# Optimization experiments

Hardware: AMD Instinct MI355X
Metric: run time of the kernel (lower is better)

The kernel has to match this reference:

```python
import jax, jax.numpy as jnp
import numpy as np
from jax import lax

SHIFT_SIZE = 5
PAD = SHIFT_SIZE // 2


def _chunk_shifts(C):
    # torch.chunk(x, 5, dim=1): chunk size = ceil(C/5); shift for chunk i is i - PAD
    csz = -(-C // SHIFT_SIZE)
    return jnp.arange(C) // csz - PAD  # (C,) in [-PAD, PAD]


def _shift_along_h(x, shifts):
    # x: (B,C,H,W). Equivalent of pad+chunk+roll(dim=2)+cat+narrow: per-channel
    # zero-filled shift along H (no wraparound since |shift| <= PAD).
    B, C, H, W = x.shape
    xp = jnp.pad(x, ((0, 0), (0, 0), (PAD, PAD), (0, 0)))
    c_idx = jnp.arange(C)[:, None]              # (C,1)
    h_idx = jnp.arange(H)[None, :] + PAD - shifts[:, None]  # (C,H)
    return xp[:, c_idx, h_idx, :]               # (B,C,H,W)


def _shift_along_w(x, shifts):
    return jnp.swapaxes(_shift_along_h(jnp.swapaxes(x, 2, 3), shifts), 2, 3)


def setup_inputs() -> dict:
    key = jax.random.key(0)
    ks = jax.random.split(key, 7)
    B, H, W, C, hidden = 8, 128, 128, 256, 256
    x = jax.random.normal(ks[0], (B, H * W, C), dtype=jnp.float32)
    w1 = jax.random.normal(ks[1], (hidden, C), dtype=jnp.float32) * 0.02
    b1 = jnp.zeros((hidden,), dtype=jnp.float32)
    fan_out = 3 * 3 * hidden // hidden  # groups = hidden
    dw_w = jax.random.normal(ks[2], (hidden, 1, 3, 3), dtype=jnp.float32) * np.sqrt(2.0 / fan_out)
    dw_b = jnp.zeros((hidden,), dtype=jnp.float32)
    w2 = jax.random.normal(ks[3], (C, hidden), dtype=jnp.float32) * 0.02
    b2 = jnp.zeros((C,), dtype=jnp.float32)
    return {"x": x, "H": H, "W": W, "w1": w1, "b1": b1,
            "dw_w": dw_w, "dw_b": dw_b, "w2": w2, "b2": b2}


def reference(x, H, W, w1, b1, dw_w, dw_b, w2, b2):
    B, N, C = x.shape
    shifts = _chunk_shifts(C)

    # --- shift along H, then fc1 ---
    xn = jnp.reshape(jnp.swapaxes(x, 1, 2), (B, C, H, W))
    x_s = _shift_along_h(xn, shifts)
    x_s = jnp.swapaxes(x_s.reshape(B, C, H * W), 1, 2)   # (B,N,C)
    h = x_s @ w1.T + b1                                  # (B,N,hidden)

    # --- depthwise 3x3 conv ---
    Ch = h.shape[-1]
    himg = jnp.reshape(jnp.swapaxes(h, 1, 2), (B, Ch, H, W))
    himg = lax.conv_general_dilated(
        himg, dw_w, window_strides=(1, 1), padding=((1, 1), (1, 1)),
        feature_group_count=Ch,
        dimension_numbers=("NCHW", "OIHW", "NCHW")) + dw_b[None, :, None, None]
    h = jnp.swapaxes(himg.reshape(B, Ch, H * W), 1, 2)

    h = jax.nn.gelu(h, approximate=False)

    # --- shift along W, then fc2 ---
    hn = jnp.reshape(jnp.swapaxes(h, 1, 2), (B, Ch, H, W))
    h_s = _shift_along_w(hn, _chunk_shifts(Ch))
    h_s = jnp.swapaxes(h_s.reshape(B, Ch, H * W), 1, 2)  # (B,N,hidden)
    out = h_s @ w2.T + b2                                # (B,N,C)
    return out
```

## Files before the change

### kernel.cpp

```cpp
#include <hip/hip_runtime.h>
#include <hip/hip_bf16.h>
#include <math.h>

#define Hc   128
#define Wc   128
#define Cc   256
#define Nc   (Hc * Wc)
#define Bn   8
#define Mtot (Bn * Nc)
#define CSZ  52
#define SPAD 2

typedef unsigned short ushort4v __attribute__((ext_vector_type(4)));
typedef unsigned short ushort8  __attribute__((ext_vector_type(8)));
typedef __bf16         bf16x8   __attribute__((ext_vector_type(8)));
typedef float          f32x4    __attribute__((ext_vector_type(4)));

__device__ __forceinline__ float bf2f(unsigned short u) {
    return __uint_as_float(((unsigned)u) << 16);
}
__device__ __forceinline__ unsigned short f2bf(float f) {
    unsigned u = __float_as_uint(f);
    return (unsigned short)((u + 0x7fffu + ((u >> 16) & 1u)) >> 16);
}
__device__ __forceinline__ unsigned pk2bf(float a, float b) {
    unsigned ua = __float_as_uint(a) + 0x8000u;
    unsigned ub = __float_as_uint(b) + 0x8000u;
    return __builtin_amdgcn_perm(ub, ua, 0x07060302);
}
__device__ __forceinline__ void async16(const void* g, void* l) {
    __builtin_amdgcn_global_load_lds(
        (const __attribute__((address_space(1))) unsigned*)g,
        (__attribute__((address_space(3))) unsigned*)l, 16, 0, 0);
}

#define FENCE(vm) asm volatile("s_waitcnt vmcnt(" #vm ") lgkmcnt(0)\n\ts_barrier" ::: "memory")

__global__ __launch_bounds__(256)
void shiftwprep_kernel(const float* __restrict__ x, unsigned short* __restrict__ xb,
                       const float* __restrict__ w1, const float* __restrict__ w2,
                       const float* __restrict__ dw_w,
                       unsigned short* __restrict__ w1b, unsigned short* __restrict__ w2b,
                       float* __restrict__ dwT)
{
    const int gid0 = blockIdx.x * 256 + threadIdx.x;
    if (blockIdx.x < 64) {
        const int g = gid0;
        {
            float4 a = *(const float4*)(w1 + (size_t)g * 4);
            ushort4v o = { f2bf(a.x), f2bf(a.y), f2bf(a.z), f2bf(a.w) };
            *(ushort4v*)(w1b + (size_t)g * 4) = o;
        }
        {
            float4 a = *(const float4*)(w2 + (size_t)g * 4);
            ushort4v o = { f2bf(a.x), f2bf(a.y), f2bf(a.z), f2bf(a.w) };
            *(ushort4v*)(w2b + (size_t)g * 4) = o;
        }
        if (g < 9 * Cc) dwT[(g % 9) * Cc + g / 9] = dw_w[g];
    }
#pragma unroll
    for (int it = 0; it < 4; ++it) {
        const int gid = gid0 + it * (4096 * 256);
        const int row = gid >> 5;
        const int c   = (gid & 31) * 8;
        const int hh  = (row >> 7) & 127;
        const int s0  = c / CSZ - SPAD;
        const int s1  = (c + 4) / CSZ - SPAD;
        const int h0  = hh - s0, h1r = hh - s1;
        float4 v0 = make_float4(0.f, 0.f, 0.f, 0.f);
        float4 v1 = make_float4(0.f, 0.f, 0.f, 0.f);
        if (h0  >= 0 && h0  < Hc)
            v0 = *(const float4*)(x + ((size_t)row + (size_t)(h0 - hh) * Wc) * Cc + c);
        if (h1r >= 0 && h1r < Hc)
            v1 = *(const float4*)(x + ((size_t)row + (size_t)(h1r - hh) * Wc) * Cc + c + 4);
        uint4 o;
        o.x = pk2bf(v0.x, v0.y); o.y = pk2bf(v0.z, v0.w);
        o.z = pk2bf(v1.x, v1.y); o.w = pk2bf(v1.z, v1.w);
        *(uint4*)(xb + (size_t)row * Cc + c) = o;
    }
}

__global__ __launch_bounds__(256)
void fc1_mfma_kernel(const unsigned short* __restrict__ xb, const unsigned short* __restrict__ w1b,
                     const float* __restrict__ b1, unsigned short* __restrict__ h1)
{
    __shared__ __align__(16) unsigned char smem[49152];
    __bf16* base = (__bf16*)smem;
    unsigned short* Cs = (unsigned short*)smem;

    const int tid  = threadIdx.x;
    const int lane = tid & 63;
    const int wave = tid >> 6;
    const int wm = (wave >> 1) * 64, wn = (wave & 1) * 64;

    const int lid = ((blockIdx.x & 7) << 8) | (blockIdx.x >> 3);
    const int bx  = lid >> 1;
    const int j0  = (lid & 1) * 128;
    const size_t m0 = (size_t)bx * 128;
    const int idx0 = tid, idx1 = tid + 256;

    const size_t aro0 = (m0 + (idx0 >> 2)) * Cc + (idx0 & 3) * 8;
    const size_t aro1 = (m0 + (idx1 >> 2)) * Cc + (idx1 & 3) * 8;
    const size_t bro0 = (size_t)(j0 + (idx0 >> 2)) * Cc + (idx0 & 3) * 8;
    const size_t bro1 = (size_t)(j0 + (idx1 >> 2)) * Cc + (idx1 & 3) * 8;

    auto stage = [&](int buf, int t) {
        const int k0 = t * 32;
        __bf16* adst = base + buf * 8192;
        __bf16* bdst = adst + 4096;
        async16(xb  + aro0 + k0, adst + idx0 * 8);
        async16(xb  + aro1 + k0, adst + idx1 * 8);
        async16(w1b + bro0 + k0, bdst + idx0 * 8);
        async16(w1b + bro1 + k0, bdst + idx1 * 8);
    };

    f32x4 acc[4][4] = {};
    const int kq = (lane >> 4) * 8;
    const int rr = lane & 15;

    stage(0, 0);
    stage(1, 1);
    FENCE(4);

#define G1_STEP(T, FN)                                                        \
    {                                                                          \
        if constexpr ((T) <= 5) stage(((T) + 2) % 3, (T) + 2);                 \
        bf16x8 a[4], b[4];                                                     \
        const __bf16* ap = base + ((T) % 3) * 8192;                            \
        const __bf16* bp = ap + 4096;                                          \
        _Pragma("unroll")                                                      \
        for (int i = 0; i < 4; ++i) {                                          \
            a[i] = *(const bf16x8*)(ap + (wm + i * 16 + rr) * 32 + kq);        \
            b[i] = *(const bf16x8*)(bp + (wn + i * 16 + rr) * 32 + kq);        \
        }                                                                      \
        _Pragma("unroll")                                                      \
        for (int i = 0; i < 4; ++i)                                            \
            _Pragma("unroll")                                                  \
            for (int j = 0; j < 4; ++j)                                        \
                acc[i][j] = __builtin_amdgcn_mfma_f32_16x16x32_bf16(a[i], b[j], acc[i][j], 0, 0, 0); \
        FN;                                                                    \
    }

    G1_STEP(0, FENCE(4));
    G1_STEP(1, FENCE(4));
    G1_STEP(2, FENCE(4));
    G1_STEP(3, FENCE(4));
    G1_STEP(4, FENCE(4));
    G1_STEP(5, FENCE(4));
    G1_STEP(6, FENCE(0));
    G1_STEP(7, __syncthreads());
#undef G1_STEP

    const int cq = (lane >> 4) * 4;
    const int cc = lane & 15;
    float bv[4];
#pragma unroll
    for (int j = 0; j < 4; ++j) bv[j] = b1[j0 + wn + j * 16 + cc];
#pragma unroll
    for (int i = 0; i < 4; ++i)
#pragma unroll
        for (int j = 0; j < 4; ++j) {
            const int col = wn + j * 16 + cc;
#pragma unroll
            for (int rg = 0; rg < 4; ++rg)
                Cs[(wm + i * 16 + cq + rg) * 136 + col] = f2bf(acc[i][j][rg] + bv[j]);
        }
    __syncthreads();
    {
        const int row = tid >> 1, hf = tid & 1;
        const unsigned short* src = Cs + row * 136 + hf * 64;
        unsigned short* dst = h1 + (m0 + row) * Cc + j0 + hf * 64;
#pragma unroll
        for (int i = 0; i < 8; ++i)
            *(uint4*)(dst + i * 8) = *(const uint4*)(src + i * 8);
    }
}

__global__ __launch_bounds__(256)
void dwconv_gelu_scatter_kernel(const unsigned short* __restrict__ h1,
                                const float* __restrict__ dwT, const float* __restrict__ dw_b,
                                unsigned short* __restrict__ gsh)
{
    const int t   = threadIdx.x;
    const int bh  = blockIdx.x;
    const int bb  = bh >> 7, hh = bh & 127;
    const size_t rowb = (size_t)bb * Nc + (size_t)hh * Wc;

    {
        const int wi = t >> 6;
        const int w  = (wi & 2) ? (wi + 124) : wi;
        const int c8 = (t & 63) * 4;
        uint2 z; z.x = 0u; z.y = 0u;
        *(uint2*)(gsh + (rowb + w) * Cc + c8) = z;
    }
    __syncthreads();

    const int cg  = t & 31;
    const int wq  = t >> 5;
    const int c0  = cg * 8;
    const int s0  = c0 / CSZ - SPAD;
    const int s1  = (c0 + 4) / CSZ - SPAD;

#pragma unroll 1
    for (int qtr = 0; qtr < 4; ++qtr) {
        const int wbase = qtr * 32 + wq * 4 - 1;

        float acc[4][8];
        {
            float4 a0 = *(const float4*)(dw_b + c0);
            float4 a1 = *(const float4*)(dw_b + c0 + 4);
#pragma unroll
            for (int i = 0; i < 4; ++i) {
                acc[i][0] = a0.x; acc[i][1] = a0.y; acc[i][2] = a0.z; acc[i][3] = a0.w;
                acc[i][4] = a1.x; acc[i][5] = a1.y; acc[i][6] = a1.z; acc[i][7] = a1.w;
            }
        }

#pragma unroll
        for (int dy = -1; dy <= 1; ++dy) {
            const int y = hh + dy;
            if (y < 0 || y >= Hc) continue;
            const unsigned short* rp = h1 + ((size_t)bb * Nc + (size_t)y * Wc) * Cc + c0;
            float in[6][8];
#pragma unroll
            for (int dx = 0; dx < 6; ++dx) {
                const int w = wbase + dx;
                ushort8 raw = {0, 0, 0, 0, 0, 0, 0, 0};
                if (w >= 0 && w < Wc) raw = *(const ushort8*)(rp + (size_t)w * Cc);
#pragma unroll
                for (int c = 0; c < 8; ++c) in[dx][c] = bf2f(raw[c]);
            }
            const float* wrow = dwT + (dy + 1) * 3 * Cc + c0;
            float wr[3][8];
#pragma unroll
            for (int tx = 0; tx < 3; ++tx) {
                float4 wa = *(const float4*)(wrow + tx * Cc);
                float4 wb = *(const float4*)(wrow + tx * Cc + 4);
                wr[tx][0] = wa.x; wr[tx][1] = wa.y; wr[tx][2] = wa.z; wr[tx][3] = wa.w;
                wr[tx][4] = wb.x; wr[tx][5] = wb.y; wr[tx][6] = wb.z; wr[tx][7] = wb.w;
            }
#pragma unroll
            for (int i = 0; i < 4; ++i)
#pragma unroll
                for (int tx = 0; tx < 3; ++tx)
#pragma unroll
                    for (int c = 0; c < 8; ++c)
                        acc[i][c] += in[i + tx][c] * wr[tx][c];
        }

#pragma unroll
        for (int i = 0; i < 4; ++i) {
            float g[8];
#pragma unroll
            for (int c = 0; c < 8; ++c) {
                const float v = acc[i][c];
                const float u = v * v;
                const float a = __builtin_fmaf(0.0713548162f, u, 1.5957691216f);
                const float e = __expf(v * a);
                g[c] = v * e * __builtin_amdgcn_rcpf(e + 1.0f);
            }
            uint2 lo, hi;
            lo.x = pk2bf(g[0], g[1]); lo.y = pk2bf(g[2], g[3]);
            hi.x = pk2bf(g[4], g[5]); hi.y = pk2bf(g[6], g[7]);
            const int wo = wbase + 1 + i;
            const int w0 = wo + s0, w1 = wo + s1;
            if ((unsigned)w0 < (unsigned)Wc) *(uint2*)(gsh + (rowb + w0) * Cc + c0)     = lo;
            if ((unsigned)w1 < (unsigned)Wc) *(uint2*)(gsh + (rowb + w1) * Cc + c0 + 4) = hi;
        }
    }
}

__global__ __launch_bounds__(256)
void fc2_mfma_kernel(const unsigned short* __restrict__ A, const unsigned short* __restrict__ w2b,
                     const float* __restrict__ b2, float* __restrict__ out)
{
    __shared__ __align__(16) unsigned char smem[49152];
    __bf16* base = (__bf16*)smem;

    const int tid  = threadIdx.x;
    const int lane = tid & 63;
    const int wave = tid >> 6;
    const int wm = (wave >> 1) * 64, wn = (wave & 1) * 64;

    const int lid = ((blockIdx.x & 7) << 8) | (blockIdx.x >> 3);
    const size_t m0 = (size_t)(lid >> 1) * 128;
    const int j0 = (lid & 1) * 128;
    const int idx0 = tid, idx1 = tid + 256;

    const size_t aro0 = (m0 + (idx0 >> 2)) * Cc + (idx0 & 3) * 8;
    const size_t aro1 = (m0 + (idx1 >> 2)) * Cc + (idx1 & 3) * 8;
    const size_t bro0 = (size_t)(j0 + (idx0 >> 2)) * Cc + (idx0 & 3) * 8;
    const size_t bro1 = (size_t)(j0 + (idx1 >> 2)) * Cc + (idx1 & 3) * 8;

    auto stage = [&](int buf, int t) {
        const int k0 = t * 32;
        __bf16* adst = base + buf * 8192;
        __bf16* bdst = adst + 4096;
        async16(A   + aro0 + k0, adst + idx0 * 8);
        async16(A   + aro1 + k0, adst + idx1 * 8);
        async16(w2b + bro0 + k0, bdst + idx0 * 8);
        async16(w2b + bro1 + k0, bdst + idx1 * 8);
    };

    f32x4 acc[4][4] = {};
    const int kq = (lane >> 4) * 8;
    const int rr = lane & 15;

    stage(0, 0);
    stage(1, 1);
    FENCE(4);

#define G2_STEP(T, FN)                                                        \
    {                                                                          \
        if constexpr ((T) <= 5) stage(((T) + 2) % 3, (T) + 2);                 \
        bf16x8 a[4], b[4];                                                     \
        const __bf16* ap = base + ((T) % 3) * 8192;                            \
        const __bf16* bp = ap + 4096;                                          \
        _Pragma("unroll")                                                      \
        for (int i = 0; i < 4; ++i) {                                          \
            a[i] = *(const bf16x8*)(ap + (wm + i * 16 + rr) * 32 + kq);        \
            b[i] = *(const bf16x8*)(bp + (wn + i * 16 + rr) * 32 + kq);        \
        }                                                                      \
        _Pragma("unroll")                                                      \
        for (int i = 0; i < 4; ++i)                                            \
            _Pragma("unroll")                                                  \
            for (int j = 0; j < 4; ++j)                                        \
                acc[i][j] = __builtin_amdgcn_mfma_f32_16x16x32_bf16(a[i], b[j], acc[i][j], 0, 0, 0); \
        FN;                                                                    \
    }

    G2_STEP(0, FENCE(4));
    G2_STEP(1, FENCE(4));
    G2_STEP(2, FENCE(4));
    G2_STEP(3, FENCE(4));
    G2_STEP(4, FENCE(4));
    G2_STEP(5, FENCE(4));
    G2_STEP(6, FENCE(0));
    G2_STEP(7, ;);
#undef G2_STEP

    const int cq = (lane >> 4) * 4;
    const int cc = lane & 15;
    float bv[4];
#pragma unroll
    for (int j = 0; j < 4; ++j) bv[j] = b2[j0 + wn + j * 16 + cc];
#pragma unroll
    for (int i = 0; i < 4; ++i)
#pragma unroll
        for (int j = 0; j < 4; ++j) {
            const int col = j0 + wn + j * 16 + cc;
#pragma unroll
            for (int rg = 0; rg < 4; ++rg)
                out[(m0 + wm + i * 16 + cq + rg) * Cc + col] = acc[i][j][rg] + bv[j];
        }
}

extern "C" void kernel_launch(void* const* d_in, const int* in_sizes, int n_in,
                              void* d_out, int out_size, void* d_ws, size_t ws_size,
                              hipStream_t stream) {
    const float* x    = (const float*)d_in[0];
    const float* w1   = (const float*)d_in[3];
    const float* b1   = (const float*)d_in[4];
    const float* dw_w = (const float*)d_in[5];
    const float* dw_b = (const float*)d_in[6];
    const float* w2   = (const float*)d_in[7];
    const float* b2   = (const float*)d_in[8];
    float* out = (float*)d_out;

    unsigned short* h1  = (unsigned short*)d_ws;
    unsigned short* gsh = h1 + (size_t)Mtot * Cc;
    unsigned short* w1b = gsh + (size_t)Mtot * Cc;
    unsigned short* w2b = w1b + 65536;
    float*          dwT = (float*)(w2b + 65536);

    shiftwprep_kernel<<<dim3(4096), dim3(256), 0, stream>>>(x, gsh, w1, w2, dw_w, w1b, w2b, dwT);
    fc1_mfma_kernel<<<dim3(2 * Mtot / 128), dim3(256), 0, stream>>>(gsh, w1b, b1, h1);
    dwconv_gelu_scatter_kernel<<<dim3(Mtot / 128), dim3(256), 0, stream>>>(h1, dwT, dw_b, gsh);
    fc2_mfma_kernel<<<dim3(2 * Mtot / 128), dim3(256), 0, stream>>>(gsh, w2b, b2, out);
}
```

Baseline: 350.2 us.

## Widen GEMM tiles to full N=256 and XOR-swizzle LDS staging

Both fc1 and fc2 GEMM kernels now compute a 128x256 output tile per block, so each block covers all output columns. This halves the grid and means the A operand is loaded from global memory only once instead of twice. The LDS layout for A and B is XOR-swizzled on 16-byte chunks to reduce bank conflicts on the fragment reads. The trade-off is twice the accumulator registers (4x8 f32x4 per wave) and 72KB of LDS per block, which lowers occupancy; the fc1 epilogue now writes its output in two passes through the LDS buffer.

```diff
diff --git a/kernel.cpp b/kernel.cpp
--- a/kernel.cpp
+++ b/kernel.cpp
@@ -84,95 +84,110 @@
 void fc1_mfma_kernel(const unsigned short* __restrict__ xb, const unsigned short* __restrict__ w1b,
                      const float* __restrict__ b1, unsigned short* __restrict__ h1)
 {
-    __shared__ __align__(16) unsigned char smem[49152];
-    __bf16* base = (__bf16*)smem;
-    unsigned short* Cs = (unsigned short*)smem;
+    __shared__ __align__(16) unsigned char sm[73728];
+    unsigned short* Cs = (unsigned short*)sm;
 
     const int tid  = threadIdx.x;
     const int lane = tid & 63;
     const int wave = tid >> 6;
-    const int wm = (wave >> 1) * 64, wn = (wave & 1) * 64;
-
-    const int lid = ((blockIdx.x & 7) << 8) | (blockIdx.x >> 3);
-    const int bx  = lid >> 1;
-    const int j0  = (lid & 1) * 128;
-    const size_t m0 = (size_t)bx * 128;
-    const int idx0 = tid, idx1 = tid + 256;
-
-    const size_t aro0 = (m0 + (idx0 >> 2)) * Cc + (idx0 & 3) * 8;
-    const size_t aro1 = (m0 + (idx1 >> 2)) * Cc + (idx1 & 3) * 8;
-    const size_t bro0 = (size_t)(j0 + (idx0 >> 2)) * Cc + (idx0 & 3) * 8;
-    const size_t bro1 = (size_t)(j0 + (idx1 >> 2)) * Cc + (idx1 & 3) * 8;
+    const int wm = (wave >> 1) * 64;
+    const int wn = (wave & 1) * 128;
+
+    const int lid = ((blockIdx.x & 7) << 7) | (blockIdx.x >> 3);
+    const size_t m0 = (size_t)lid * 128;
+
+    const int qa0 = tid, qa1 = tid + 256;
+    const int ra0 = qa0 >> 2, ra1 = qa1 >> 2;
+    const size_t aof0 = (m0 + ra0) * Cc + (((qa0 & 3) ^ (ra0 & 3)) << 3);
+    const size_t aof1 = (m0 + ra1) * Cc + (((qa1 & 3) ^ (ra1 & 3)) << 3);
+    const int qb0 = tid, qb1 = tid + 256, qb2 = tid + 512, qb3 = tid + 768;
+    const int rb0 = qb0 >> 2, rb1 = qb1 >> 2, rb2 = qb2 >> 2, rb3 = qb3 >> 2;
+    const int bof0 = rb0 * Cc + (((qb0 & 3) ^ (rb0 & 3)) << 3);
+    const int bof1 = rb1 * Cc + (((qb1 & 3) ^ (rb1 & 3)) << 3);
+    const int bof2 = rb2 * Cc + (((qb2 & 3) ^ (rb2 & 3)) << 3);
+    const int bof3 = rb3 * Cc + (((qb3 & 3) ^ (rb3 & 3)) << 3);
 
     auto stage = [&](int buf, int t) {
         const int k0 = t * 32;
-        __bf16* adst = base + buf * 8192;
-        __bf16* bdst = adst + 4096;
-        async16(xb  + aro0 + k0, adst + idx0 * 8);
-        async16(xb  + aro1 + k0, adst + idx1 * 8);
-        async16(w1b + bro0 + k0, bdst + idx0 * 8);
-        async16(w1b + bro1 + k0, bdst + idx1 * 8);
+        unsigned char* ad = sm + buf * 24576;
+        unsigned char* bd = ad + 8192;
+        async16(xb  + aof0 + k0, ad + qa0 * 16);
+        async16(xb  + aof1 + k0, ad + qa1 * 16);
+        async16(w1b + bof0 + k0, bd + qb0 * 16);
+        async16(w1b + bof1 + k0, bd + qb1 * 16);
+        async16(w1b + bof2 + k0, bd + qb2 * 16);
+        async16(w1b + bof3 + k0, bd + qb3 * 16);
     };
 
-    f32x4 acc[4][4] = {};
-    const int kq = (lane >> 4) * 8;
-    const int rr = lane & 15;
+    f32x4 acc[4][8] = {};
+    const int rr  = lane & 15;
+    const int axo = (((lane >> 4) ^ (rr & 3)) << 3);
 
     stage(0, 0);
     stage(1, 1);
-    FENCE(4);
+    FENCE(6);
 
 #define G1_STEP(T, FN)                                                        \
     {                                                                          \
         if constexpr ((T) <= 5) stage(((T) + 2) % 3, (T) + 2);                 \
-        bf16x8 a[4], b[4];                                                     \
-        const __bf16* ap = base + ((T) % 3) * 8192;                            \
-        const __bf16* bp = ap + 4096;                                          \
-        _Pragma("unroll")                                                      \
-        for (int i = 0; i < 4; ++i) {                                          \
-            a[i] = *(const bf16x8*)(ap + (wm + i * 16 + rr) * 32 + kq);        \
-            b[i] = *(const bf16x8*)(bp + (wn + i * 16 + rr) * 32 + kq);        \
-        }                                                                      \
+        const __bf16* ap = (const __bf16*)(sm + ((T) % 3) * 24576);            \
+        const __bf16* bp = (const __bf16*)(sm + ((T) % 3) * 24576 + 8192);     \
+        bf16x8 a[4];                                                           \
         _Pragma("unroll")                                                      \
         for (int i = 0; i < 4; ++i)                                            \
+            a[i] = *(const bf16x8*)(ap + (wm + i * 16 + rr) * 32 + axo);       \
+        _Pragma("unroll")                                                      \
+        for (int jh = 0; jh < 2; ++jh) {                                       \
+            bf16x8 b[4];                                                       \
             _Pragma("unroll")                                                  \
             for (int j = 0; j < 4; ++j)                                        \
-                acc[i][j] = __builtin_amdgcn_mfma_f32_16x16x32_bf16(a[i], b[j], acc[i][j], 0, 0, 0); \
+                b[j] = *(const bf16x8*)(bp + (wn + jh * 64 + j * 16 + rr) * 32 + axo); \
+            _Pragma("unroll")                                                  \
+            for (int i = 0; i < 4; ++i)                                        \
+                _Pragma("unroll")                                              \
+                for (int j = 0; j < 4; ++j)                                    \
+                    acc[i][jh * 4 + j] = __builtin_amdgcn_mfma_f32_16x16x32_bf16(a[i], b[j], acc[i][jh * 4 + j], 0, 0, 0); \
+        }                                                                      \
         FN;                                                                    \
     }
 
-    G1_STEP(0, FENCE(4));
-    G1_STEP(1, FENCE(4));
-    G1_STEP(2, FENCE(4));
-    G1_STEP(3, FENCE(4));
-    G1_STEP(4, FENCE(4));
-    G1_STEP(5, FENCE(4));
+    G1_STEP(0, FENCE(6));
+    G1_STEP(1, FENCE(6));
+    G1_STEP(2, FENCE(6));
+    G1_STEP(3, FENCE(6));
+    G1_STEP(4, FENCE(6));
+    G1_STEP(5, FENCE(6));
     G1_STEP(6, FENCE(0));
-    G1_STEP(7, __syncthreads());
+    G1_STEP(7, ;);
 #undef G1_STEP
 
-    const int cq = (lane >> 4) * 4;
-    const int cc = lane & 15;
-    float bv[4];
-#pragma unroll
-    for (int j = 0; j < 4; ++j) bv[j] = b1[j0 + wn + j * 16 + cc];
-#pragma unroll
-    for (int i = 0; i < 4; ++i)
-#pragma unroll
-        for (int j = 0; j < 4; ++j) {
-            const int col = wn + j * 16 + cc;
-#pragma unroll
-            for (int rg = 0; rg < 4; ++rg)
-                Cs[(wm + i * 16 + cq + rg) * 136 + col] = f2bf(acc[i][j][rg] + bv[j]);
-        }
-    __syncthreads();
-    {
-        const int row = tid >> 1, hf = tid & 1;
-        const unsigned short* src = Cs + row * 136 + hf * 64;
-        unsigned short* dst = h1 + (m0 + row) * Cc + j0 + hf * 64;
-#pragma unroll
-        for (int i = 0; i < 8; ++i)
-            *(uint4*)(dst + i * 8) = *(const uint4*)(src + i * 8);
+    const int cq  = (lane >> 4) * 4;
+    const int cc  = lane & 15;
+    const int lcb = wn >> 1;
+#pragma unroll
+    for (int p = 0; p < 2; ++p) {
+        __syncthreads();
+        float bv[4];
+#pragma unroll
+        for (int j = 0; j < 4; ++j) bv[j] = b1[wn + p * 64 + j * 16 + cc];
+#pragma unroll
+        for (int i = 0; i < 4; ++i)
+#pragma unroll
+            for (int j = 0; j < 4; ++j) {
+                const int col = lcb + j * 16 + cc;
+#pragma unroll
+                for (int rg = 0; rg < 4; ++rg)
+                    Cs[(wm + i * 16 + cq + rg) * 136 + col] = f2bf(acc[i][p * 4 + j][rg] + bv[j]);
+            }
+        __syncthreads();
+        {
+            const int row = tid >> 1, hf = tid & 1;
+            const unsigned short* src = Cs + row * 136 + hf * 64;
+            unsigned short* dst = h1 + (m0 + row) * Cc + (hf * 2 + p) * 64;
+#pragma unroll
+            for (int i = 0; i < 8; ++i)
+                *(uint4*)(dst + i * 8) = *(const uint4*)(src + i * 8);
+        }
     }
 }
 
@@ -274,84 +289,96 @@
 void fc2_mfma_kernel(const unsigned short* __restrict__ A, const unsigned short* __restrict__ w2b,
                      const float* __restrict__ b2, float* __restrict__ out)
 {
-    __shared__ __align__(16) unsigned char smem[49152];
-    __bf16* base = (__bf16*)smem;
+    __shared__ __align__(16) unsigned char sm[73728];
 
     const int tid  = threadIdx.x;
     const int lane = tid & 63;
     const int wave = tid >> 6;
-    const int wm = (wave >> 1) * 64, wn = (wave & 1) * 64;
-
-    const int lid = ((blockIdx.x & 7) << 8) | (blockIdx.x >> 3);
-    const size_t m0 = (size_t)(lid >> 1) * 128;
-    const int j0 = (lid & 1) * 128;
-    const int idx0 = tid, idx1 = tid + 256;
-
-    const size_t aro0 = (m0 + (idx0 >> 2)) * Cc + (idx0 & 3) * 8;
-    const size_t aro1 = (m0 + (idx1 >> 2)) * Cc + (idx1 & 3) * 8;
-    const size_t bro0 = (size_t)(j0 + (idx0 >> 2)) * Cc + (idx0 & 3) * 8;
-    const size_t bro1 = (size_t)(j0 + (idx1 >> 2)) * Cc + (idx1 & 3) * 8;
+    const int wm = (wave >> 1) * 64;
+    const int wn = (wave & 1) * 128;
+
+    const int lid = ((blockIdx.x & 7) << 7) | (blockIdx.x >> 3);
+    const size_t m0 = (size_t)lid * 128;
+
+    const int qa0 = tid, qa1 = tid + 256;
+    const int ra0 = qa0 >> 2, ra1 = qa1 >> 2;
+    const size_t aof0 = (m0 + ra0) * Cc + (((qa0 & 3) ^ (ra0 & 3)) << 3);
+    const size_t aof1 = (m0 + ra1) * Cc + (((qa1 & 3) ^ (ra1 & 3)) << 3);
+    const int qb0 = tid, qb1 = tid + 256, qb2 = tid + 512, qb3 = tid + 768;
+    const int rb0 = qb0 >> 2, rb1 = qb1 >> 2, rb2 = qb2 >> 2, rb3 = qb3 >> 2;
+    const int bof0 = rb0 * Cc + (((qb0 & 3) ^ (rb0 & 3)) << 3);
+    const int bof1 = rb1 * Cc + (((qb1 & 3) ^ (rb1 & 3)) << 3);
+    const int bof2 = rb2 * Cc + (((qb2 & 3) ^ (rb2 & 3)) << 3);
+    const int bof3 = rb3 * Cc + (((qb3 & 3) ^ (rb3 & 3)) << 3);
 
     auto stage = [&](int buf, int t) {
         const int k0 = t * 32;
-        __bf16* adst = base + buf * 8192;
-        __bf16* bdst = adst + 4096;
-        async16(A   + aro0 + k0, adst + idx0 * 8);
-        async16(A   + aro1 + k0, adst + idx1 * 8);
-        async16(w2b + bro0 + k0, bdst + idx0 * 8);
-        async16(w2b + bro1 + k0, bdst + idx1 * 8);
+        unsigned char* ad = sm + buf * 24576;
+        unsigned char* bd = ad + 8192;
+        async16(A   + aof0 + k0, ad + qa0 * 16);
+        async16(A   + aof1 + k0, ad + qa1 * 16);
+        async16(w2b + bof0 + k0, bd + qb0 * 16);
+        async16(w2b + bof1 + k0, bd + qb1 * 16);
+        async16(w2b + bof2 + k0, bd + qb2 * 16);
+        async16(w2b + bof3 + k0, bd + qb3 * 16);
     };
 
-    f32x4 acc[4][4] = {};
-    const int kq = (lane >> 4) * 8;
-    const int rr = lane & 15;
+    f32x4 acc[4][8] = {};
+    const int rr  = lane & 15;
+    const int axo = (((lane >> 4) ^ (rr & 3)) << 3);
 
     stage(0, 0);
     stage(1, 1);
-    FENCE(4);
+    FENCE(6);
 
 #define G2_STEP(T, FN)                                                        \
     {                                                                          \
         if constexpr ((T) <= 5) stage(((T) + 2) % 3, (T) + 2);                 \
-        bf16x8 a[4], b[4];                                                     \
-        const __bf16* ap = base + ((T) % 3) * 8192;                            \
-        const __bf16* bp = ap + 4096;                                          \
-        _Pragma("unroll")                                                      \
-        for (int i = 0; i < 4; ++i) {                                          \
-            a[i] = *(const bf16x8*)(ap + (wm + i * 16 + rr) * 32 + kq);        \
-            b[i] = *(const bf16x8*)(bp + (wn + i * 16 + rr) * 32 + kq);        \
-        }                                                                      \
+        const __bf16* ap = (const __bf16*)(sm + ((T) % 3) * 24576);            \
+        const __bf16* bp = (const __bf16*)(sm + ((T) % 3) * 24576 + 8192);     \
+        bf16x8 a[4];                                                           \
         _Pragma("unroll")                                                      \
         for (int i = 0; i < 4; ++i)                                            \
+            a[i] = *(const bf16x8*)(ap + (wm + i * 16 + rr) * 32 + axo);       \
+        _Pragma("unroll")                                                      \
+        for (int jh = 0; jh < 2; ++jh) {                                       \
+            bf16x8 b[4];                                                       \
             _Pragma("unroll")                                                  \
             for (int j = 0; j < 4; ++j)                                        \
-                acc[i][j] = __builtin_amdgcn_mfma_f32_16x16x32_bf16(a[i], b[j], acc[i][j], 0, 0, 0); \
+                b[j] = *(const bf16x8*)(bp + (wn + jh * 64 + j * 16 + rr) * 32 + axo); \
+            _Pragma("unroll")                                                  \
+            for (int i = 0; i < 4; ++i)                                        \
+                _Pragma("unroll")                                              \
+                for (int j = 0; j < 4; ++j)                                    \
+                    acc[i][jh * 4 + j] = __builtin_amdgcn_mfma_f32_16x16x32_bf16(a[i], b[j], acc[i][jh * 4 + j], 0, 0, 0); \
+        }                                                                      \
         FN;                                                                    \
     }
 
-    G2_STEP(0, FENCE(4));
-    G2_STEP(1, FENCE(4));
-    G2_STEP(2, FENCE(4));
-    G2_STEP(3, FENCE(4));
-    G2_STEP(4, FENCE(4));
-    G2_STEP(5, FENCE(4));
+    G2_STEP(0, FENCE(6));
+    G2_STEP(1, FENCE(6));
+    G2_STEP(2, FENCE(6));
+    G2_STEP(3, FENCE(6));
+    G2_STEP(4, FENCE(6));
+    G2_STEP(5, FENCE(6));
     G2_STEP(6, FENCE(0));
     G2_STEP(7, ;);
 #undef G2_STEP
 
     const int cq = (lane >> 4) * 4;
     const int cc = lane & 15;
-    float bv[4];
-#pragma unroll
-    for (int j = 0; j < 4; ++j) bv[j] = b2[j0 + wn + j * 16 + cc];
+    float bv[8];
+#pragma unroll
+    for (int jj = 0; jj < 8; ++jj)
+        bv[jj] = b2[wn + (jj >> 2) * 64 + (jj & 3) * 16 + cc];
 #pragma unroll
     for (int i = 0; i < 4; ++i)
 #pragma unroll
-        for (int j = 0; j < 4; ++j) {
-            const int col = j0 + wn + j * 16 + cc;
+        for (int jj = 0; jj < 8; ++jj) {
+            const int col = wn + (jj >> 2) * 64 + (jj & 3) * 16 + cc;
 #pragma unroll
             for (int rg = 0; rg < 4; ++rg)
-                out[(m0 + wm + i * 16 + cq + rg) * Cc + col] = acc[i][j][rg] + bv[j];
+                out[(m0 + wm + i * 16 + cq + rg) * Cc + col] = acc[i][jj][rg] + bv[jj];
         }
 }
 
@@ -374,7 +401,7 @@
     float*          dwT = (float*)(w2b + 65536);
 
     shiftwprep_kernel<<<dim3(4096), dim3(256), 0, stream>>>(x, gsh, w1, w2, dw_w, w1b, w2b, dwT);
-    fc1_mfma_kernel<<<dim3(2 * Mtot / 128), dim3(256), 0, stream>>>(gsh, w1b, b1, h1);
+    fc1_mfma_kernel<<<dim3(Mtot / 128), dim3(256), 0, stream>>>(gsh, w1b, b1, h1);
     dwconv_gelu_scatter_kernel<<<dim3(Mtot / 128), dim3(256), 0, stream>>>(h1, dwT, dw_b, gsh);
-    fc2_mfma_kernel<<<dim3(2 * Mtot / 128), dim3(256), 0, stream>>>(gsh, w2b, b2, out);
-}
+    fc2_mfma_kernel<<<dim3(Mtot / 128), dim3(256), 0, stream>>>(gsh, w2b, b2, out);
+}
```

Result: no change. 349.3 us (-0.2%).
